# Performance work log

Hardware: AMD Instinct MI355X
Metric: run time of the kernel (lower is better)

## Reference

```python
import jax, jax.numpy as jnp
import numpy as np

T, H, E, I, K = 2048, 2048, 16, 512, 2
ROUTED_SCALE = 1.5   # config.moe_router_scaling_factor
SWIGLU_LIMIT = 7.0   # config.swiglu_limits[layer_id]


def setup_inputs() -> dict:
    key = jax.random.key(0)
    k1, k2, k3, k4, k5 = jax.random.split(key, 5)
    hidden_states = jax.random.normal(k1, (T, H), jnp.float32)
    gate_w = jax.random.normal(k2, (E, H), jnp.float32) * 0.02
    router_bias = jax.random.normal(k3, (E,), jnp.float32) * 0.01
    w13 = jax.random.normal(k4, (E, 2 * I, H), jnp.float32) * 0.02  # [gate; up] fused
    w2 = jax.random.normal(k5, (E, H, I), jnp.float32) * 0.02
    return {"hidden_states": hidden_states, "gate_w": gate_w,
            "router_bias": router_bias, "w13": w13, "w2": w2, "top_k": K}


def reference(hidden_states, gate_w, router_bias, w13, w2, top_k):
    n_tok = hidden_states.shape[0]
    n_exp = gate_w.shape[0]
    # fp32 gate (need_fp32_gate=True)
    router_logits = hidden_states.astype(jnp.float32) @ gate_w.T          # [T, E]
    scores = jax.nn.sigmoid(router_logits)
    # correction bias only affects expert choice, not the combine weights
    _, topk_ids = jax.lax.top_k(scores + router_bias[None, :], top_k)     # [T, K]
    topk_w = jnp.take_along_axis(scores, topk_ids, axis=1)                # [T, K]
    topk_w = topk_w / jnp.sum(topk_w, axis=1, keepdims=True)              # renormalize
    topk_w = topk_w * ROUTED_SCALE
    # scatter routing weights into dense per-expert combine weights [T, E]
    comb = jnp.zeros((n_tok, n_exp), jnp.float32)
    comb = comb.at[jnp.arange(n_tok)[:, None], topk_ids].add(topk_w)
    # expert SwiGLU MLPs, dense over experts (zero combine weight == not routed)
    gu = jnp.einsum('th,eoh->teo', hidden_states, w13)                    # [T, E, 2I]
    g, u = jnp.split(gu, 2, axis=-1)
    g = jnp.minimum(g, SWIGLU_LIMIT)                                      # gemm1_clamp_limit
    u = jnp.clip(u, -SWIGLU_LIMIT, SWIGLU_LIMIT)
    act = g * jax.nn.sigmoid(g) * u                                       # silu(gate) * up
    expert_out = jnp.einsum('tei,ehi->teh', act, w2)                      # [T, E, H]
    return jnp.einsum('teh,te->th', expert_out, comb)                     # [T, H]
```

## Files before the change

### kernel.cpp

```cpp
#include <hip/hip_runtime.h>
#include <hip/hip_bf16.h>
#include <math.h>

#define T_TOK 2048
#define H_DIM 2048
#define E_EXP 16
#define I_DIM 512
#define TWO_I 1024
#define ROUTED_SCALE 1.5f
#define SWIGLU_LIMIT 7.0f

#define BM 64
#define KC 64
#define MAX_TILES 80

typedef __attribute__((ext_vector_type(8))) short bf16x8;
typedef __attribute__((ext_vector_type(4))) float f32x4;
typedef unsigned short u16;

__device__ inline u16 f2bf(float f) {
    return __builtin_bit_cast(u16, __float2bfloat16(f));
}
__device__ inline ushort4 pack4(float4 a) {
    ushort4 v;
    v.x = f2bf(a.x); v.y = f2bf(a.y); v.z = f2bf(a.z); v.w = f2bf(a.w);
    return v;
}

__device__ inline void gload16(const u16* g, u16* l) {
    __builtin_amdgcn_global_load_lds(
        (const __attribute__((address_space(1))) void*)(g),
        (__attribute__((address_space(3))) void*)(l), 16, 0, 0);
}

#define SWZ(row, k) ((row) * 64 + ((k) ^ (((row) & 7) << 3)))

__global__ __launch_bounds__(256) void router_kernel(
    const float* __restrict__ hs, const float* __restrict__ gw,
    const float* __restrict__ bias, int* cnt, int* tok_list, float* w_list,
    u16* __restrict__ hs_bf)
{
    int wave = threadIdx.x >> 6;
    int lane = threadIdx.x & 63;
    int t = blockIdx.x * 4 + wave;
    if (t >= T_TOK) return;
    const float* x = hs + (size_t)t * H_DIM;

    float acc[E_EXP];
#pragma unroll
    for (int e = 0; e < E_EXP; ++e) acc[e] = 0.f;

#pragma unroll 2
    for (int c = 0; c < 8; ++c) {
        int col = c * 256 + lane * 4;
        float4 xv = *(const float4*)(x + col);
        *(ushort4*)(hs_bf + (size_t)t * H_DIM + col) = pack4(xv);
#pragma unroll
        for (int e = 0; e < E_EXP; ++e) {
            float4 gv = *(const float4*)(gw + (size_t)e * H_DIM + col);
            acc[e] = fmaf(xv.x, gv.x, acc[e]);
            acc[e] = fmaf(xv.y, gv.y, acc[e]);
            acc[e] = fmaf(xv.z, gv.z, acc[e]);
            acc[e] = fmaf(xv.w, gv.w, acc[e]);
        }
    }
#pragma unroll
    for (int e = 0; e < E_EXP; ++e) {
        for (int m = 32; m >= 1; m >>= 1)
            acc[e] += __shfl_xor(acc[e], m, 64);
    }
    if (lane == 0) {
        float sc[E_EXP], bsc[E_EXP];
#pragma unroll
        for (int e = 0; e < E_EXP; ++e) {
            sc[e] = 1.f / (1.f + expf(-acc[e]));
            bsc[e] = sc[e] + bias[e];
        }
        int e0 = 0; float b0 = bsc[0];
#pragma unroll
        for (int e = 1; e < E_EXP; ++e) if (bsc[e] > b0) { b0 = bsc[e]; e0 = e; }
        int e1 = -1; float b1 = -1e30f;
#pragma unroll
        for (int e = 0; e < E_EXP; ++e) {
            if (e == e0) continue;
            if (bsc[e] > b1) { b1 = bsc[e]; e1 = e; }
        }
        float s0 = sc[e0], s1 = sc[e1];
        float inv = ROUTED_SCALE / (s0 + s1);
        int p0 = atomicAdd(&cnt[e0], 1);
        tok_list[e0 * T_TOK + p0] = t;
        w_list[e0 * T_TOK + p0] = s0 * inv;
        int p1 = atomicAdd(&cnt[e1], 1);
        tok_list[e1 * T_TOK + p1] = t;
        w_list[e1 * T_TOK + p1] = s1 * inv;
    }
}

__global__ void scatter_build(const int* __restrict__ cnt,
    const int* __restrict__ tok_list, const float* __restrict__ w_list,
    int* A_tok, float* A_w, int* tile_e, int* tile_r0)
{
    int c[E_EXP], offs[E_EXP + 1];
    offs[0] = 0;
#pragma unroll
    for (int e = 0; e < E_EXP; ++e) {
        c[e] = cnt[e];
        offs[e + 1] = offs[e] + ((c[e] + BM - 1) & ~(BM - 1));
    }
    int idx = blockIdx.x * 256 + threadIdx.x;
    int e = idx >> 11;
    int pos = idx & (T_TOK - 1);
    int ce = c[e];
    int pe = (ce + BM - 1) & ~(BM - 1);
    if (pos < ce) {
        A_tok[offs[e] + pos] = tok_list[idx];
        A_w[offs[e] + pos] = w_list[idx];
    } else if (pos < pe) {
        A_tok[offs[e] + pos] = -1;
        A_w[offs[e] + pos] = 0.f;
    }
    if (idx == 0) {
        int nt = 0;
        for (int ee = 0; ee < E_EXP; ++ee) {
            int ntile = (c[ee] + BM - 1) >> 6;
            for (int j = 0; j < ntile; ++j) {
                tile_e[nt] = ee;
                tile_r0[nt] = offs[ee] + j * BM;
                ++nt;
            }
        }
        for (; nt < MAX_TILES; ++nt) tile_e[nt] = -1;
    }
}

__global__ __launch_bounds__(256, 3) void gemm1_act(
    const u16* __restrict__ hs_bf, const float* __restrict__ w13,
    const int* __restrict__ A_tok, const int* __restrict__ tile_e,
    const int* __restrict__ tile_r0, u16* __restrict__ act)
{
    int b = blockIdx.x;
    int id = (b & 7) * 80 + (b >> 3);
    int tile = id % MAX_TILES;
    int y = id / MAX_TILES;
    int e = tile_e[tile];
    if (e < 0) return;
    int row0 = tile_r0[tile];
    int i0 = y * 64;
    int tid = threadIdx.x;

    __shared__ u16 Xs[2][4096];
    __shared__ u16 Gs[2][4096];
    __shared__ u16 Us[2][4096];

    const int l = tid & 63, w = tid >> 6;

    const int rlo = l >> 3;
    const int c8 = (l & 7) << 3;
    const int ksrc = c8 ^ (rlo << 3);
    const int rowA = w * 16 + rlo;
    const int rowB = rowA + 8;
    int tokA = A_tok[row0 + rowA]; if (tokA < 0) tokA = 0;
    int tokB = A_tok[row0 + rowB]; if (tokB < 0) tokB = 0;
    const u16* sXA = hs_bf + (size_t)tokA * H_DIM + ksrc;
    const u16* sXB = hs_bf + (size_t)tokB * H_DIM + ksrc;
    const int dA = w * 1024;

#define X_STAGE(bb, t) do { int ko = (t) * KC; \
    gload16(sXA + ko, &Xs[bb][dA]);  gload16(sXB + ko, &Xs[bb][dA + 512]); } while (0)

    const int srow = tid >> 4;
    const int sc4  = tid & 15;
    const int kphys = (sc4 * 4) ^ ((srow & 7) << 3);
    const int sbase = srow * 64 + kphys;
    const float* gsrc = w13 + ((size_t)e * TWO_I + i0 + srow) * H_DIM + sc4 * 4;
    const float* usrc = gsrc + (size_t)I_DIM * H_DIM;

    float4 gld[4], uld[4];
#define W_LOAD(t) do { int k0 = (t) * KC; \
    gld[0] = *(const float4*)(gsrc + k0); \
    gld[1] = *(const float4*)(gsrc + k0 + 16 * H_DIM); \
    gld[2] = *(const float4*)(gsrc + k0 + 32 * H_DIM); \
    gld[3] = *(const float4*)(gsrc + k0 + 48 * H_DIM); \
    uld[0] = *(const float4*)(usrc + k0); \
    uld[1] = *(const float4*)(usrc + k0 + 16 * H_DIM); \
    uld[2] = *(const float4*)(usrc + k0 + 32 * H_DIM); \
    uld[3] = *(const float4*)(usrc + k0 + 48 * H_DIM); } while (0)

#define W_WRITE(bb) do { \
    *(ushort4*)&Gs[bb][sbase]        = pack4(gld[0]); \
    *(ushort4*)&Gs[bb][sbase + 1024] = pack4(gld[1]); \
    *(ushort4*)&Gs[bb][sbase + 2048] = pack4(gld[2]); \
    *(ushort4*)&Gs[bb][sbase + 3072] = pack4(gld[3]); \
    *(ushort4*)&Us[bb][sbase]        = pack4(uld[0]); \
    *(ushort4*)&Us[bb][sbase + 1024] = pack4(uld[1]); \
    *(ushort4*)&Us[bb][sbase + 2048] = pack4(uld[2]); \
    *(ushort4*)&Us[bb][sbase + 3072] = pack4(uld[3]); } while (0)

    const int wm = w >> 1, wn = w & 1;
    const int lr = l & 15;
    const int lg = l >> 4;
    const int ra0 = wm * 32 + lr, ra1 = ra0 + 16;
    const int rb0 = wn * 32 + lr, rb1 = rb0 + 16;
    int ia0[2], ia1[2], ib0[2], ib1[2];
#pragma unroll
    for (int kh = 0; kh < 2; ++kh) {
        int e2 = kh * 32 + lg * 8;
        ia0[kh] = SWZ(ra0, e2); ia1[kh] = SWZ(ra1, e2);
        ib0[kh] = SWZ(rb0, e2); ib1[kh] = SWZ(rb1, e2);
    }

    const f32x4 Z4 = {0.f, 0.f, 0.f, 0.f};
    f32x4 aG[2][2], aU[2][2];
#pragma unroll
    for (int m = 0; m < 2; ++m)
#pragma unroll
        for (int n = 0; n < 2; ++n) { aG[m][n] = Z4; aU[m][n] = Z4; }

    W_LOAD(0);
    X_STAGE(0, 0);
    W_WRITE(0);
    __syncthreads();
    int cur = 0;
    const int NT = H_DIM / KC;
    for (int t = 0; t < NT; ++t) {
        const bool more = (t + 1 < NT);
        if (more) {
            X_STAGE(cur ^ 1, t + 1);
            W_LOAD(t + 1);
            __builtin_amdgcn_sched_barrier(0);
        }
#pragma unroll
        for (int kh = 0; kh < 2; ++kh) {
            bf16x8 a0 = *(const bf16x8*)&Xs[cur][ia0[kh]];
            bf16x8 a1 = *(const bf16x8*)&Xs[cur][ia1[kh]];
            bf16x8 g0 = *(const bf16x8*)&Gs[cur][ib0[kh]];
            bf16x8 g1 = *(const bf16x8*)&Gs[cur][ib1[kh]];
            bf16x8 u0 = *(const bf16x8*)&Us[cur][ib0[kh]];
            bf16x8 u1 = *(const bf16x8*)&Us[cur][ib1[kh]];
            aG[0][0] = __builtin_amdgcn_mfma_f32_16x16x32_bf16(a0, g0, aG[0][0], 0, 0, 0);
            aG[0][1] = __builtin_amdgcn_mfma_f32_16x16x32_bf16(a0, g1, aG[0][1], 0, 0, 0);
            aG[1][0] = __builtin_amdgcn_mfma_f32_16x16x32_bf16(a1, g0, aG[1][0], 0, 0, 0);
            aG[1][1] = __builtin_amdgcn_mfma_f32_16x16x32_bf16(a1, g1, aG[1][1], 0, 0, 0);
            aU[0][0] = __builtin_amdgcn_mfma_f32_16x16x32_bf16(a0, u0, aU[0][0], 0, 0, 0);
            aU[0][1] = __builtin_amdgcn_mfma_f32_16x16x32_bf16(a0, u1, aU[0][1], 0, 0, 0);
            aU[1][0] = __builtin_amdgcn_mfma_f32_16x16x32_bf16(a1, u0, aU[1][0], 0, 0, 0);
            aU[1][1] = __builtin_amdgcn_mfma_f32_16x16x32_bf16(a1, u1, aU[1][1], 0, 0, 0);
        }
        if (more) W_WRITE(cur ^ 1);
        __syncthreads();
        cur ^= 1;
    }
#undef X_STAGE
#undef W_LOAD
#undef W_WRITE

#pragma unroll
    for (int m = 0; m < 2; ++m)
#pragma unroll
        for (int n = 0; n < 2; ++n) {
            int col = i0 + wn * 32 + n * 16 + lr;
            int rbase = row0 + wm * 32 + m * 16 + lg * 4;
#pragma unroll
            for (int q = 0; q < 4; ++q) {
                float g = fminf(aG[m][n][q], SWIGLU_LIMIT);
                float u = fminf(fmaxf(aU[m][n][q], -SWIGLU_LIMIT), SWIGLU_LIMIT);
                float s = 1.f / (1.f + __expf(-g));
                act[(size_t)(rbase + q) * I_DIM + col] = f2bf(g * s * u);
            }
        }
}

__global__ __launch_bounds__(256, 3) void gemm2_scatter(
    const u16* __restrict__ act, const float* __restrict__ w2,
    const int* __restrict__ A_tok, const float* __restrict__ A_w,
    const int* __restrict__ tile_e, const int* __restrict__ tile_r0,
    float* __restrict__ out)
{
    int b = blockIdx.x;
    int id = (b & 7) * 320 + (b >> 3);
    int tile = id % MAX_TILES;
    int y = id / MAX_TILES;
    int e = tile_e[tile];
    if (e < 0) return;
    int row0 = tile_r0[tile];
    int h0 = y * 64;
    int tid = threadIdx.x;

    __shared__ u16 As[2][4096];
    __shared__ u16 Bs[2][4096];
    __shared__ int toks[BM];
    __shared__ float wts[BM];
    if (tid < BM) { toks[tid] = A_tok[row0 + tid]; wts[tid] = A_w[row0 + tid]; }

    const int l = tid & 63, w = tid >> 6;

    const int rlo = l >> 3;
    const int c8 = (l & 7) << 3;
    const int ksrc = c8 ^ (rlo << 3);
    const int rowA = w * 16 + rlo;
    const int rowB = rowA + 8;
    const u16* sAA = act + (size_t)(row0 + rowA) * I_DIM + ksrc;
    const u16* sAB = act + (size_t)(row0 + rowB) * I_DIM + ksrc;
    const int dA = w * 1024;

#define A_STAGE(bb, t) do { int ko = (t) * KC; \
    gload16(sAA + ko, &As[bb][dA]);  gload16(sAB + ko, &As[bb][dA + 512]); } while (0)

    const int srow = tid >> 4;
    const int sc4  = tid & 15;
    const int kphys = (sc4 * 4) ^ ((srow & 7) << 3);
    const int sbase = srow * 64 + kphys;
    const float* bsrc = w2 + ((size_t)e * H_DIM + h0 + srow) * I_DIM + sc4 * 4;

    float4 bld[4];
#define B_LOAD(t) do { int k0 = (t) * KC; \
    bld[0] = *(const float4*)(bsrc + k0); \
    bld[1] = *(const float4*)(bsrc + k0 + 16 * I_DIM); \
    bld[2] = *(const float4*)(bsrc + k0 + 32 * I_DIM); \
    bld[3] = *(const float4*)(bsrc + k0 + 48 * I_DIM); } while (0)

#define B_WRITE(bb) do { \
    *(ushort4*)&Bs[bb][sbase]        = pack4(bld[0]); \
    *(ushort4*)&Bs[bb][sbase + 1024] = pack4(bld[1]); \
    *(ushort4*)&Bs[bb][sbase + 2048] = pack4(bld[2]); \
    *(ushort4*)&Bs[bb][sbase + 3072] = pack4(bld[3]); } while (0)

    const int wm = w >> 1, wn = w & 1;
    const int lr = l & 15;
    const int lg = l >> 4;
    const int ra0 = wm * 32 + lr, ra1 = ra0 + 16;
    const int rb0 = wn * 32 + lr, rb1 = rb0 + 16;
    int ia0[2], ia1[2], ib0[2], ib1[2];
#pragma unroll
    for (int kh = 0; kh < 2; ++kh) {
        int e2 = kh * 32 + lg * 8;
        ia0[kh] = SWZ(ra0, e2); ia1[kh] = SWZ(ra1, e2);
        ib0[kh] = SWZ(rb0, e2); ib1[kh] = SWZ(rb1, e2);
    }

    const f32x4 Z4 = {0.f, 0.f, 0.f, 0.f};
    f32x4 acc[2][2];
#pragma unroll
    for (int m = 0; m < 2; ++m)
#pragma unroll
        for (int n = 0; n < 2; ++n) acc[m][n] = Z4;

    B_LOAD(0);
    A_STAGE(0, 0);
    B_WRITE(0);
    __syncthreads();
    int cur = 0;
    const int NT = I_DIM / KC;
    for (int t = 0; t < NT; ++t) {
        const bool more = (t + 1 < NT);
        if (more) {
            A_STAGE(cur ^ 1, t + 1);
            B_LOAD(t + 1);
            __builtin_amdgcn_sched_barrier(0);
        }
#pragma unroll
        for (int kh = 0; kh < 2; ++kh) {
            bf16x8 a0 = *(const bf16x8*)&As[cur][ia0[kh]];
            bf16x8 a1 = *(const bf16x8*)&As[cur][ia1[kh]];
            bf16x8 b0 = *(const bf16x8*)&Bs[cur][ib0[kh]];
            bf16x8 b1 = *(const bf16x8*)&Bs[cur][ib1[kh]];
            acc[0][0] = __builtin_amdgcn_mfma_f32_16x16x32_bf16(a0, b0, acc[0][0], 0, 0, 0);
            acc[0][1] = __builtin_amdgcn_mfma_f32_16x16x32_bf16(a0, b1, acc[0][1], 0, 0, 0);
            acc[1][0] = __builtin_amdgcn_mfma_f32_16x16x32_bf16(a1, b0, acc[1][0], 0, 0, 0);
            acc[1][1] = __builtin_amdgcn_mfma_f32_16x16x32_bf16(a1, b1, acc[1][1], 0, 0, 0);
        }
        if (more) B_WRITE(cur ^ 1);
        __syncthreads();
        cur ^= 1;
    }
#undef A_STAGE
#undef B_LOAD
#undef B_WRITE

#pragma unroll
    for (int m = 0; m < 2; ++m)
#pragma unroll
        for (int n = 0; n < 2; ++n) {
            int col = h0 + wn * 32 + n * 16 + lr;
            int sbase2 = wm * 32 + m * 16 + lg * 4;
#pragma unroll
            for (int q = 0; q < 4; ++q) {
                int slot = sbase2 + q;
                int tok = toks[slot];
                if (tok >= 0)
                    atomicAdd(&out[(size_t)tok * H_DIM + col], acc[m][n][q] * wts[slot]);
            }
        }
}

extern "C" void kernel_launch(void* const* d_in, const int* in_sizes, int n_in,
                              void* d_out, int out_size, void* d_ws, size_t ws_size,
                              hipStream_t stream) {
    const float* hs   = (const float*)d_in[0];
    const float* gw   = (const float*)d_in[1];
    const float* bias = (const float*)d_in[2];
    const float* w13  = (const float*)d_in[3];
    const float* w2   = (const float*)d_in[4];
    float* out = (float*)d_out;

    char* ws = (char*)d_ws;
    int*   cnt      = (int*)(ws + 0);
    int*   tile_e   = (int*)(ws + 64);
    int*   tile_r0  = (int*)(ws + 384);
    int*   tok_list = (int*)(ws + 1024);
    float* w_list   = (float*)(ws + 132096);
    int*   A_tok    = (int*)(ws + 263168);
    float* A_w      = (float*)(ws + 283648);
    u16*   act      = (u16*)(ws + 304128);
    u16*   hs_bf    = (u16*)(ws + 5547008);

    hipMemsetAsync(d_out, 0, (size_t)T_TOK * H_DIM * sizeof(float), stream);
    hipMemsetAsync(cnt, 0, 64, stream);

    router_kernel<<<T_TOK / 4, 256, 0, stream>>>(hs, gw, bias, cnt, tok_list, w_list, hs_bf);
    scatter_build<<<(E_EXP * T_TOK) / 256, 256, 0, stream>>>(cnt, tok_list, w_list, A_tok, A_w, tile_e, tile_r0);

    gemm1_act<<<MAX_TILES * 8, 256, 0, stream>>>(hs_bf, w13, A_tok, tile_e, tile_r0, act);
    gemm2_scatter<<<MAX_TILES * 32, 256, 0, stream>>>(act, w2, A_tok, A_w, tile_e, tile_r0, out);
}
```

Measured before the change: 178.0 us.

## Deepen weight prefetch to two stages with manual waitcnt barriers in both GEMMs

Both expert GEMM kernels now keep two register sets of fp32 weight loads in flight, so global loads for tile t+2 are issued while tile t is computed. The loop is unrolled by two with explicit s_waitcnt vmcnt/lgkmcnt and raw s_barrier in place of __syncthreads, aiming to hide global-memory latency. gemm2 also drops the shared token/weight staging, reading A_tok/A_w directly in the epilogue, and raises its launch-bounds occupancy hint from 3 to 4. The cost is more registers per thread and hand-tuned wait counts that have to match the exact number of outstanding loads. The tail iterations re-load the clamped last tile, which is redundant work.

```diff
diff --git a/kernel.cpp b/kernel.cpp
--- a/kernel.cpp
+++ b/kernel.cpp
@@ -32,6 +32,7 @@
         (const __attribute__((address_space(1))) void*)(g),
         (__attribute__((address_space(3))) void*)(l), 16, 0, 0);
 }
+#define SCHED0() __builtin_amdgcn_sched_barrier(0)
 
 #define SWZ(row, k) ((row) * 64 + ((k) ^ (((row) & 7) << 3)))
 
@@ -175,26 +176,26 @@
     const float* gsrc = w13 + ((size_t)e * TWO_I + i0 + srow) * H_DIM + sc4 * 4;
     const float* usrc = gsrc + (size_t)I_DIM * H_DIM;
 
-    float4 gld[4], uld[4];
-#define W_LOAD(t) do { int k0 = (t) * KC; \
-    gld[0] = *(const float4*)(gsrc + k0); \
-    gld[1] = *(const float4*)(gsrc + k0 + 16 * H_DIM); \
-    gld[2] = *(const float4*)(gsrc + k0 + 32 * H_DIM); \
-    gld[3] = *(const float4*)(gsrc + k0 + 48 * H_DIM); \
-    uld[0] = *(const float4*)(usrc + k0); \
-    uld[1] = *(const float4*)(usrc + k0 + 16 * H_DIM); \
-    uld[2] = *(const float4*)(usrc + k0 + 32 * H_DIM); \
-    uld[3] = *(const float4*)(usrc + k0 + 48 * H_DIM); } while (0)
-
-#define W_WRITE(bb) do { \
-    *(ushort4*)&Gs[bb][sbase]        = pack4(gld[0]); \
-    *(ushort4*)&Gs[bb][sbase + 1024] = pack4(gld[1]); \
-    *(ushort4*)&Gs[bb][sbase + 2048] = pack4(gld[2]); \
-    *(ushort4*)&Gs[bb][sbase + 3072] = pack4(gld[3]); \
-    *(ushort4*)&Us[bb][sbase]        = pack4(uld[0]); \
-    *(ushort4*)&Us[bb][sbase + 1024] = pack4(uld[1]); \
-    *(ushort4*)&Us[bb][sbase + 2048] = pack4(uld[2]); \
-    *(ushort4*)&Us[bb][sbase + 3072] = pack4(uld[3]); } while (0)
+    float4 gA[4], uA[4], gB[4], uB[4];
+#define W_LOAD(S, t) do { int k0 = (t) * KC; \
+    g##S[0] = *(const float4*)(gsrc + k0); \
+    g##S[1] = *(const float4*)(gsrc + k0 + 16 * H_DIM); \
+    g##S[2] = *(const float4*)(gsrc + k0 + 32 * H_DIM); \
+    g##S[3] = *(const float4*)(gsrc + k0 + 48 * H_DIM); \
+    u##S[0] = *(const float4*)(usrc + k0); \
+    u##S[1] = *(const float4*)(usrc + k0 + 16 * H_DIM); \
+    u##S[2] = *(const float4*)(usrc + k0 + 32 * H_DIM); \
+    u##S[3] = *(const float4*)(usrc + k0 + 48 * H_DIM); } while (0)
+
+#define W_WRITE(S, bb) do { \
+    *(ushort4*)&Gs[bb][sbase]        = pack4(g##S[0]); \
+    *(ushort4*)&Gs[bb][sbase + 1024] = pack4(g##S[1]); \
+    *(ushort4*)&Gs[bb][sbase + 2048] = pack4(g##S[2]); \
+    *(ushort4*)&Gs[bb][sbase + 3072] = pack4(g##S[3]); \
+    *(ushort4*)&Us[bb][sbase]        = pack4(u##S[0]); \
+    *(ushort4*)&Us[bb][sbase + 1024] = pack4(u##S[1]); \
+    *(ushort4*)&Us[bb][sbase + 2048] = pack4(u##S[2]); \
+    *(ushort4*)&Us[bb][sbase + 3072] = pack4(u##S[3]); } while (0)
 
     const int wm = w >> 1, wn = w & 1;
     const int lr = l & 15;
@@ -216,43 +217,64 @@
 #pragma unroll
         for (int n = 0; n < 2; ++n) { aG[m][n] = Z4; aU[m][n] = Z4; }
 
-    W_LOAD(0);
+#define MFMA_STEP(c) do { \
+    _Pragma("unroll") for (int kh = 0; kh < 2; ++kh) { \
+        bf16x8 a0 = *(const bf16x8*)&Xs[c][ia0[kh]]; \
+        bf16x8 a1 = *(const bf16x8*)&Xs[c][ia1[kh]]; \
+        bf16x8 g0 = *(const bf16x8*)&Gs[c][ib0[kh]]; \
+        bf16x8 g1 = *(const bf16x8*)&Gs[c][ib1[kh]]; \
+        bf16x8 u0 = *(const bf16x8*)&Us[c][ib0[kh]]; \
+        bf16x8 u1 = *(const bf16x8*)&Us[c][ib1[kh]]; \
+        aG[0][0] = __builtin_amdgcn_mfma_f32_16x16x32_bf16(a0, g0, aG[0][0], 0, 0, 0); \
+        aG[0][1] = __builtin_amdgcn_mfma_f32_16x16x32_bf16(a0, g1, aG[0][1], 0, 0, 0); \
+        aG[1][0] = __builtin_amdgcn_mfma_f32_16x16x32_bf16(a1, g0, aG[1][0], 0, 0, 0); \
+        aG[1][1] = __builtin_amdgcn_mfma_f32_16x16x32_bf16(a1, g1, aG[1][1], 0, 0, 0); \
+        aU[0][0] = __builtin_amdgcn_mfma_f32_16x16x32_bf16(a0, u0, aU[0][0], 0, 0, 0); \
+        aU[0][1] = __builtin_amdgcn_mfma_f32_16x16x32_bf16(a0, u1, aU[0][1], 0, 0, 0); \
+        aU[1][0] = __builtin_amdgcn_mfma_f32_16x16x32_bf16(a1, u0, aU[1][0], 0, 0, 0); \
+        aU[1][1] = __builtin_amdgcn_mfma_f32_16x16x32_bf16(a1, u1, aU[1][1], 0, 0, 0); \
+    } } while (0)
+
+    const int NT = H_DIM / KC;
     X_STAGE(0, 0);
-    W_WRITE(0);
-    __syncthreads();
-    int cur = 0;
-    const int NT = H_DIM / KC;
-    for (int t = 0; t < NT; ++t) {
-        const bool more = (t + 1 < NT);
-        if (more) {
-            X_STAGE(cur ^ 1, t + 1);
-            W_LOAD(t + 1);
-            __builtin_amdgcn_sched_barrier(0);
-        }
-#pragma unroll
-        for (int kh = 0; kh < 2; ++kh) {
-            bf16x8 a0 = *(const bf16x8*)&Xs[cur][ia0[kh]];
-            bf16x8 a1 = *(const bf16x8*)&Xs[cur][ia1[kh]];
-            bf16x8 g0 = *(const bf16x8*)&Gs[cur][ib0[kh]];
-            bf16x8 g1 = *(const bf16x8*)&Gs[cur][ib1[kh]];
-            bf16x8 u0 = *(const bf16x8*)&Us[cur][ib0[kh]];
-            bf16x8 u1 = *(const bf16x8*)&Us[cur][ib1[kh]];
-            aG[0][0] = __builtin_amdgcn_mfma_f32_16x16x32_bf16(a0, g0, aG[0][0], 0, 0, 0);
-            aG[0][1] = __builtin_amdgcn_mfma_f32_16x16x32_bf16(a0, g1, aG[0][1], 0, 0, 0);
-            aG[1][0] = __builtin_amdgcn_mfma_f32_16x16x32_bf16(a1, g0, aG[1][0], 0, 0, 0);
-            aG[1][1] = __builtin_amdgcn_mfma_f32_16x16x32_bf16(a1, g1, aG[1][1], 0, 0, 0);
-            aU[0][0] = __builtin_amdgcn_mfma_f32_16x16x32_bf16(a0, u0, aU[0][0], 0, 0, 0);
-            aU[0][1] = __builtin_amdgcn_mfma_f32_16x16x32_bf16(a0, u1, aU[0][1], 0, 0, 0);
-            aU[1][0] = __builtin_amdgcn_mfma_f32_16x16x32_bf16(a1, u0, aU[1][0], 0, 0, 0);
-            aU[1][1] = __builtin_amdgcn_mfma_f32_16x16x32_bf16(a1, u1, aU[1][1], 0, 0, 0);
-        }
-        if (more) W_WRITE(cur ^ 1);
-        __syncthreads();
-        cur ^= 1;
+    W_LOAD(A, 0);
+    X_STAGE(1, 1);
+    W_LOAD(B, 1);
+    W_WRITE(A, 0);
+    asm volatile("s_waitcnt lgkmcnt(0)" ::: "memory");
+    SCHED0();
+    __builtin_amdgcn_s_barrier();
+
+    for (int t = 0; t < NT; t += 2) {
+        {
+            int ts = (t + 1 < NT) ? t + 1 : NT - 1;
+            int tx = (t + 2 < NT) ? t + 2 : NT - 1;
+            X_STAGE(1, ts);
+            W_LOAD(A, tx);
+            SCHED0();
+            MFMA_STEP(0);
+            W_WRITE(B, 1);
+            asm volatile("s_waitcnt vmcnt(8) lgkmcnt(0)" ::: "memory");
+            SCHED0();
+            __builtin_amdgcn_s_barrier();
+        }
+        {
+            int ts = (t + 2 < NT) ? t + 2 : NT - 1;
+            int tx = (t + 3 < NT) ? t + 3 : NT - 1;
+            X_STAGE(0, ts);
+            W_LOAD(B, tx);
+            SCHED0();
+            MFMA_STEP(1);
+            W_WRITE(A, 0);
+            asm volatile("s_waitcnt vmcnt(8) lgkmcnt(0)" ::: "memory");
+            SCHED0();
+            __builtin_amdgcn_s_barrier();
+        }
     }
 #undef X_STAGE
 #undef W_LOAD
 #undef W_WRITE
+#undef MFMA_STEP
 
 #pragma unroll
     for (int m = 0; m < 2; ++m)
@@ -270,7 +292,7 @@
         }
 }
 
-__global__ __launch_bounds__(256, 3) void gemm2_scatter(
+__global__ __launch_bounds__(256, 4) void gemm2_scatter(
     const u16* __restrict__ act, const float* __restrict__ w2,
     const int* __restrict__ A_tok, const float* __restrict__ A_w,
     const int* __restrict__ tile_e, const int* __restrict__ tile_r0,
@@ -288,9 +310,6 @@
 
     __shared__ u16 As[2][4096];
     __shared__ u16 Bs[2][4096];
-    __shared__ int toks[BM];
-    __shared__ float wts[BM];
-    if (tid < BM) { toks[tid] = A_tok[row0 + tid]; wts[tid] = A_w[row0 + tid]; }
 
     const int l = tid & 63, w = tid >> 6;
 
@@ -312,18 +331,18 @@
     const int sbase = srow * 64 + kphys;
     const float* bsrc = w2 + ((size_t)e * H_DIM + h0 + srow) * I_DIM + sc4 * 4;
 
-    float4 bld[4];
-#define B_LOAD(t) do { int k0 = (t) * KC; \
-    bld[0] = *(const float4*)(bsrc + k0); \
-    bld[1] = *(const float4*)(bsrc + k0 + 16 * I_DIM); \
-    bld[2] = *(const float4*)(bsrc + k0 + 32 * I_DIM); \
-    bld[3] = *(const float4*)(bsrc + k0 + 48 * I_DIM); } while (0)
-
-#define B_WRITE(bb) do { \
-    *(ushort4*)&Bs[bb][sbase]        = pack4(bld[0]); \
-    *(ushort4*)&Bs[bb][sbase + 1024] = pack4(bld[1]); \
-    *(ushort4*)&Bs[bb][sbase + 2048] = pack4(bld[2]); \
-    *(ushort4*)&Bs[bb][sbase + 3072] = pack4(bld[3]); } while (0)
+    float4 bA[4], bB[4];
+#define B_LOAD(S, t) do { int k0 = (t) * KC; \
+    b##S[0] = *(const float4*)(bsrc + k0); \
+    b##S[1] = *(const float4*)(bsrc + k0 + 16 * I_DIM); \
+    b##S[2] = *(const float4*)(bsrc + k0 + 32 * I_DIM); \
+    b##S[3] = *(const float4*)(bsrc + k0 + 48 * I_DIM); } while (0)
+
+#define B_WRITE(S, bb) do { \
+    *(ushort4*)&Bs[bb][sbase]        = pack4(b##S[0]); \
+    *(ushort4*)&Bs[bb][sbase + 1024] = pack4(b##S[1]); \
+    *(ushort4*)&Bs[bb][sbase + 2048] = pack4(b##S[2]); \
+    *(ushort4*)&Bs[bb][sbase + 3072] = pack4(b##S[3]); } while (0)
 
     const int wm = w >> 1, wn = w & 1;
     const int lr = l & 15;
@@ -345,37 +364,58 @@
 #pragma unroll
         for (int n = 0; n < 2; ++n) acc[m][n] = Z4;
 
-    B_LOAD(0);
+#define MFMA_STEP(c) do { \
+    _Pragma("unroll") for (int kh = 0; kh < 2; ++kh) { \
+        bf16x8 a0 = *(const bf16x8*)&As[c][ia0[kh]]; \
+        bf16x8 a1 = *(const bf16x8*)&As[c][ia1[kh]]; \
+        bf16x8 b0 = *(const bf16x8*)&Bs[c][ib0[kh]]; \
+        bf16x8 b1 = *(const bf16x8*)&Bs[c][ib1[kh]]; \
+        acc[0][0] = __builtin_amdgcn_mfma_f32_16x16x32_bf16(a0, b0, acc[0][0], 0, 0, 0); \
+        acc[0][1] = __builtin_amdgcn_mfma_f32_16x16x32_bf16(a0, b1, acc[0][1], 0, 0, 0); \
+        acc[1][0] = __builtin_amdgcn_mfma_f32_16x16x32_bf16(a1, b0, acc[1][0], 0, 0, 0); \
+        acc[1][1] = __builtin_amdgcn_mfma_f32_16x16x32_bf16(a1, b1, acc[1][1], 0, 0, 0); \
+    } } while (0)
+
+    const int NT = I_DIM / KC;
     A_STAGE(0, 0);
-    B_WRITE(0);
-    __syncthreads();
-    int cur = 0;
-    const int NT = I_DIM / KC;
-    for (int t = 0; t < NT; ++t) {
-        const bool more = (t + 1 < NT);
-        if (more) {
-            A_STAGE(cur ^ 1, t + 1);
-            B_LOAD(t + 1);
-            __builtin_amdgcn_sched_barrier(0);
-        }
-#pragma unroll
-        for (int kh = 0; kh < 2; ++kh) {
-            bf16x8 a0 = *(const bf16x8*)&As[cur][ia0[kh]];
-            bf16x8 a1 = *(const bf16x8*)&As[cur][ia1[kh]];
-            bf16x8 b0 = *(const bf16x8*)&Bs[cur][ib0[kh]];
-            bf16x8 b1 = *(const bf16x8*)&Bs[cur][ib1[kh]];
-            acc[0][0] = __builtin_amdgcn_mfma_f32_16x16x32_bf16(a0, b0, acc[0][0], 0, 0, 0);
-            acc[0][1] = __builtin_amdgcn_mfma_f32_16x16x32_bf16(a0, b1, acc[0][1], 0, 0, 0);
-            acc[1][0] = __builtin_amdgcn_mfma_f32_16x16x32_bf16(a1, b0, acc[1][0], 0, 0, 0);
-            acc[1][1] = __builtin_amdgcn_mfma_f32_16x16x32_bf16(a1, b1, acc[1][1], 0, 0, 0);
-        }
-        if (more) B_WRITE(cur ^ 1);
-        __syncthreads();
-        cur ^= 1;
+    B_LOAD(A, 0);
+    A_STAGE(1, 1);
+    B_LOAD(B, 1);
+    B_WRITE(A, 0);
+    asm volatile("s_waitcnt lgkmcnt(0)" ::: "memory");
+    SCHED0();
+    __builtin_amdgcn_s_barrier();
+
+    for (int t = 0; t < NT; t += 2) {
+        {
+            int ts = (t + 1 < NT) ? t + 1 : NT - 1;
+            int tx = (t + 2 < NT) ? t + 2 : NT - 1;
+            A_STAGE(1, ts);
+            B_LOAD(A, tx);
+            SCHED0();
+            MFMA_STEP(0);
+            B_WRITE(B, 1);
+            asm volatile("s_waitcnt vmcnt(4) lgkmcnt(0)" ::: "memory");
+            SCHED0();
+            __builtin_amdgcn_s_barrier();
+        }
+        {
+            int ts = (t + 2 < NT) ? t + 2 : NT - 1;
+            int tx = (t + 3 < NT) ? t + 3 : NT - 1;
+            A_STAGE(0, ts);
+            B_LOAD(B, tx);
+            SCHED0();
+            MFMA_STEP(1);
+            B_WRITE(A, 0);
+            asm volatile("s_waitcnt vmcnt(4) lgkmcnt(0)" ::: "memory");
+            SCHED0();
+            __builtin_amdgcn_s_barrier();
+        }
     }
 #undef A_STAGE
 #undef B_LOAD
 #undef B_WRITE
+#undef MFMA_STEP
 
 #pragma unroll
     for (int m = 0; m < 2; ++m)
@@ -385,10 +425,10 @@
             int sbase2 = wm * 32 + m * 16 + lg * 4;
 #pragma unroll
             for (int q = 0; q < 4; ++q) {
-                int slot = sbase2 + q;
-                int tok = toks[slot];
+                int slot = row0 + sbase2 + q;
+                int tok = A_tok[slot];
                 if (tok >= 0)
-                    atomicAdd(&out[(size_t)tok * H_DIM + col], acc[m][n][q] * wts[slot]);
+                    atomicAdd(&out[(size_t)tok * H_DIM + col], acc[m][n][q] * A_w[slot]);
             }
         }
 }
```

Measured after the change: 191.9 us. +7.8%, slower.
